# Optimization experiments

Measured on AMD Instinct MI355X. Metric: run time of the kernel, lower is better.

Reference implementation:

```python
import jax, jax.numpy as jnp
import numpy as np

D, H, K = 384, 6, 8

def _ln(x, g, b, eps=1e-5):
    mu = jnp.mean(x, axis=-1, keepdims=True)
    var = jnp.mean((x - mu) ** 2, axis=-1, keepdims=True)
    return (x - mu) * jax.lax.rsqrt(var + eps) * g + b

def setup_inputs() -> dict:
    key = jax.random.key(0)
    ks = jax.random.split(key, 20)
    B, N = 4, 2048
    s = 0.02
    inp = {
        'x': jax.random.normal(ks[0], (B, N, D), jnp.float32),
        'knn_index': jax.random.randint(ks[1], (B * K * N,), 0, B * N, jnp.int64),
        'ln1_g': jnp.ones((D,), jnp.float32),
        'ln1_b': jnp.zeros((D,), jnp.float32),
        'w_qkv': jax.random.normal(ks[2], (D, 3 * D), jnp.float32) * s,
        'w_proj': jax.random.normal(ks[3], (D, D), jnp.float32) * s,
        'b_proj': jnp.zeros((D,), jnp.float32),
        'w_knn': jax.random.normal(ks[4], (2 * D, D), jnp.float32) * s,
        'b_knn': jnp.zeros((D,), jnp.float32),
        'w_g1': jax.random.normal(ks[5], (2 * D, D), jnp.float32) * s,
        'b_g1': jnp.zeros((D,), jnp.float32),
        'w_g2': jax.random.normal(ks[6], (D, D), jnp.float32) * s,
        'b_g2': jnp.zeros((D,), jnp.float32),
        'ln2_g': jnp.ones((D,), jnp.float32),
        'ln2_b': jnp.zeros((D,), jnp.float32),
        'w_fc1': jax.random.normal(ks[7], (D, 4 * D), jnp.float32) * s,
        'b_fc1': jnp.zeros((4 * D,), jnp.float32),
        'w_fc2': jax.random.normal(ks[8], (4 * D, D), jnp.float32) * s,
        'b_fc2': jnp.zeros((D,), jnp.float32),
    }
    return inp

def reference(x, knn_index, ln1_g, ln1_b, w_qkv, w_proj, b_proj, w_knn, b_knn,
              w_g1, b_g1, w_g2, b_g2, ln2_g, ln2_b, w_fc1, b_fc1, w_fc2, b_fc2):
    B, N, _ = x.shape
    hd = D // H
    scale = hd ** -0.5
    nx = _ln(x, ln1_g, ln1_b)
    # --- self attention ---
    qkv = (nx @ w_qkv).reshape(B, N, 3, H, hd).transpose(2, 0, 3, 1, 4)  # [3,B,H,N,hd]
    q, k, v = qkv[0], qkv[1], qkv[2]
    attn = jax.nn.softmax(jnp.einsum('bhnd,bhmd->bhnm', q * scale, k), axis=-1)
    attn_out = jnp.einsum('bhnm,bhmd->bhnd', attn, v).transpose(0, 2, 1, 3).reshape(B, N, D)
    attn_out = attn_out @ w_proj + b_proj
    # --- EdgeConv-style graph feature: gather-concat-MLP-maxpool ---
    feat = nx.reshape(B * N, D)[knn_index].reshape(B, K, N, D)
    xe = jnp.broadcast_to(nx[:, None], (B, K, N, D))
    gf = jnp.concatenate([feat - xe, xe], axis=-1)  # [B,K,N,2D]
    knn_out = jnp.max(jax.nn.leaky_relu(gf @ w_knn + b_knn, 0.2), axis=1)  # [B,N,D]
    # --- salience gate ---
    gi = jnp.concatenate([attn_out, knn_out], axis=-1)
    gate = jax.nn.sigmoid(jax.nn.gelu(gi @ w_g1 + b_g1, approximate=False) @ w_g2 + b_g2)
    fused = (1 - gate) * attn_out + gate * knn_out
    x = x + fused
    # --- FFN ---
    h = jax.nn.gelu(_ln(x, ln2_g, ln2_b) @ w_fc1 + b_fc1, approximate=False)
    x = x + (h @ w_fc2 + b_fc2)
    return x
```

## Files before the change

### kernel.cpp

```cpp
#include <hip/hip_runtime.h>
#include <math.h>

typedef unsigned short u16;
typedef __attribute__((ext_vector_type(8))) short short8;
typedef __attribute__((ext_vector_type(4))) float floatx4;
typedef __attribute__((ext_vector_type(16))) float floatx16;
typedef __attribute__((ext_vector_type(4))) short sh4v;
typedef __attribute__((ext_vector_type(2))) unsigned uint2v;

union sh4u { sh4v v; u16 u[4]; };
union sh8u { short8 v; u16 u[8]; };
union sh8w { short8 v; unsigned w[4]; };

__device__ __forceinline__ floatx4 mfma16(short8 a, short8 b, floatx4 c) {
  return __builtin_amdgcn_mfma_f32_16x16x32_bf16(a, b, c, 0, 0, 0);
}
__device__ __forceinline__ floatx16 mfma32(short8 a, short8 b, floatx16 c) {
  return __builtin_amdgcn_mfma_f32_32x32x16_bf16(a, b, c, 0, 0, 0);
}

__device__ __forceinline__ floatx4 zero4() {
  floatx4 z = {0.f, 0.f, 0.f, 0.f};
  return z;
}
__device__ __forceinline__ floatx16 zero16() {
  floatx16 z;
#pragma unroll
  for (int i = 0; i < 16; i++) z[i] = 0.f;
  return z;
}

__device__ __forceinline__ float hexp2(float x) {
  return __builtin_amdgcn_exp2f(x);
}

__device__ __forceinline__ u16 f2b(float f) {
  union { float f; unsigned u; } v; v.f = f;
  unsigned u = v.u;
  return (u16)((u + 0x7FFFu + ((u >> 16) & 1u)) >> 16);
}

__device__ __forceinline__ float b2f(u16 u) {
  union { unsigned u; float f; } v; v.u = ((unsigned)u) << 16;
  return v.f;
}

__device__ __forceinline__ float blo(unsigned w) {
  union { unsigned u; float f; } v; v.u = w << 16;
  return v.f;
}
__device__ __forceinline__ float bhi(unsigned w) {
  union { unsigned u; float f; } v; v.u = w & 0xFFFF0000u;
  return v.f;
}

__device__ __forceinline__ float gelu_exact(float x) {
  return 0.5f * x * (1.f + erff(x * 0.70710678118654752440f));
}

__device__ __forceinline__ unsigned pack2(float a, float b) {
  return (unsigned)f2b(a) | ((unsigned)f2b(b) << 16);
}

__device__ __forceinline__ unsigned permpack(float p0, float p1) {
  return __builtin_amdgcn_perm(__float_as_uint(p1), __float_as_uint(p0), 0x07060302u);
}

__global__ __launch_bounds__(256) void tcln_kernel(
    const float* __restrict__ p0, const float* __restrict__ p1,
    const float* __restrict__ p2, const float* __restrict__ p3,
    const float* __restrict__ p4, const float* __restrict__ p5,
    const float* __restrict__ wknn,
    u16* __restrict__ o0, u16* __restrict__ o1, u16* __restrict__ o2,
    u16* __restrict__ o3, u16* __restrict__ o4, u16* __restrict__ o5,
    u16* __restrict__ wcT,
    const float* __restrict__ x, const float* __restrict__ g,
    const float* __restrict__ bia, u16* __restrict__ nx) {
  __shared__ u16 L[64][66];
  int t = blockIdx.x, tid = threadIdx.x;
  if (t >= 612) {
    int wave = tid >> 6, lane = tid & 63;
    int row = (t - 612) * 4 + wave;
    const float* xr = x + (size_t)row * 384;
    float v[6];
    float s = 0.f;
#pragma unroll
    for (int j = 0; j < 6; j++) { v[j] = xr[lane + 64 * j]; s += v[j]; }
#pragma unroll
    for (int off = 32; off > 0; off >>= 1) s += __shfl_xor(s, off);
    float mu = s * (1.f / 384.f);
    float ss = 0.f;
#pragma unroll
    for (int j = 0; j < 6; j++) { float d = v[j] - mu; ss += d * d; }
#pragma unroll
    for (int off = 32; off > 0; off >>= 1) ss += __shfl_xor(ss, off);
    float rstd = rsqrtf(ss * (1.f / 384.f) + 1e-5f);
    u16* orow = nx + (size_t)row * 384;
#pragma unroll
    for (int j = 0; j < 6; j++) {
      int d = lane + 64 * j;
      orow[d] = f2b((v[j] - mu) * rstd * g[d] + bia[d]);
    }
    return;
  }
  if (t >= 540) {
    t -= 540;
    int tk = t / 12, tn = t % 12;
    int k0 = tk * 64, j0 = tn * 64;
#pragma unroll
    for (int i = 0; i < 4; i++) {
      int c = tid + 256 * i;
      int r = c >> 4, c4 = (c & 15) * 4;
      floatx4 v;
      if (j0 < 384) {
        v = *(const floatx4*)(wknn + (size_t)(k0 + r) * 384 + j0 + c4);
      } else {
        floatx4 a = *(const floatx4*)(wknn + (size_t)(384 + k0 + r) * 384 + (j0 - 384) + c4);
        floatx4 b = *(const floatx4*)(wknn + (size_t)(k0 + r) * 384 + (j0 - 384) + c4);
        v = a - b;
      }
      *(unsigned*)&L[r][c4]     = pack2(v[0], v[1]);
      *(unsigned*)&L[r][c4 + 2] = pack2(v[2], v[3]);
    }
    __syncthreads();
#pragma unroll
    for (int i = 0; i < 2; i++) {
      int c = tid + 256 * i;
      int nn = c >> 3, k8 = (c & 7) * 8;
      sh8u pk;
#pragma unroll
      for (int j = 0; j < 8; j++) pk.u[j] = L[k8 + j][nn];
      *(short8*)(wcT + (size_t)(j0 + nn) * 384 + k0 + k8) = pk.v;
    }
    return;
  }
  const float* src; u16* dst; int Kd, Nd, tk, tn;
  if      (t < 108) { src = p0; dst = o0; Kd = 384;  Nd = 1152; tk = t / 18; tn = t % 18; }
  else if (t < 144) { src = p1; dst = o1; Kd = 384;  Nd = 384;  t -= 108; tk = t / 6;  tn = t % 6; }
  else if (t < 216) { src = p2; dst = o2; Kd = 768;  Nd = 384;  t -= 144; tk = t / 6;  tn = t % 6; }
  else if (t < 252) { src = p3; dst = o3; Kd = 384;  Nd = 384;  t -= 216; tk = t / 6;  tn = t % 6; }
  else if (t < 396) { src = p4; dst = o4; Kd = 384;  Nd = 1536; t -= 252; tk = t / 24; tn = t % 24; }
  else              { src = p5; dst = o5; Kd = 1536; Nd = 384;  t -= 396; tk = t / 6;  tn = t % 6; }
  int k0 = tk * 64, n0 = tn * 64;
#pragma unroll
  for (int i = 0; i < 4; i++) {
    int c = tid + 256 * i;
    int r = c >> 4, c4 = (c & 15) * 4;
    floatx4 v = *(const floatx4*)(src + (size_t)(k0 + r) * Nd + n0 + c4);
    *(unsigned*)&L[r][c4]     = pack2(v[0], v[1]);
    *(unsigned*)&L[r][c4 + 2] = pack2(v[2], v[3]);
  }
  __syncthreads();
#pragma unroll
  for (int i = 0; i < 2; i++) {
    int c = tid + 256 * i;
    int nn = c >> 3, k8 = (c & 7) * 8;
    sh8u pk;
#pragma unroll
    for (int j = 0; j < 8; j++) pk.u[j] = L[k8 + j][nn];
    *(short8*)(dst + (size_t)(n0 + nn) * Kd + k0 + k8) = pk.v;
  }
}

__global__ __launch_bounds__(256) void lnb_kernel(const u16* __restrict__ x,
                                                  const float* __restrict__ g,
                                                  const float* __restrict__ bia,
                                                  u16* __restrict__ out) {
  int wave = threadIdx.x >> 6, lane = threadIdx.x & 63;
  int row = blockIdx.x * 4 + wave;
  const u16* xr = x + (size_t)row * 384;
  float v[6];
  float s = 0.f;
#pragma unroll
  for (int j = 0; j < 6; j++) { v[j] = b2f(xr[lane + 64 * j]); s += v[j]; }
#pragma unroll
  for (int off = 32; off > 0; off >>= 1) s += __shfl_xor(s, off);
  float mu = s * (1.f / 384.f);
  float ss = 0.f;
#pragma unroll
  for (int j = 0; j < 6; j++) { float d = v[j] - mu; ss += d * d; }
#pragma unroll
  for (int off = 32; off > 0; off >>= 1) ss += __shfl_xor(ss, off);
  float rstd = rsqrtf(ss * (1.f / 384.f) + 1e-5f);
  u16* orow = out + (size_t)row * 384;
#pragma unroll
  for (int j = 0; j < 6; j++) {
    int d = lane + 64 * j;
    orow[d] = f2b((v[j] - mu) * rstd * g[d] + bia[d]);
  }
}

template <int EPI>
__global__ __launch_bounds__(256) void gemm64_kernel(
    const u16* __restrict__ A0, const u16* __restrict__ A1, int Ksplit,
    const u16* __restrict__ BwT, const u16* __restrict__ BwT2, int N, int K,
    const float* __restrict__ bias,
    float* __restrict__ outF, u16* __restrict__ outB, u16* __restrict__ outB2,
    const u16* __restrict__ eA16, const u16* __restrict__ eK16,
    const float* __restrict__ eX, u16* __restrict__ outV) {
  __shared__ u16 As[64][72];
  __shared__ u16 Bs[128][72];
  int tid = threadIdx.x;
  int lane = tid & 63, w = tid >> 6, quad = lane >> 4, l16 = lane & 15;
  int n0 = blockIdx.x * 128, m0 = blockIdx.y * 64;
  int ra = tid >> 3, ca = (tid & 7) * 8;
  const u16* Bsrc = BwT;
  int nbase = n0;
  if (EPI == 8 && n0 >= 1152) { Bsrc = BwT2; nbase = n0 - 1152; }
  floatx4 acc[4][2];
#pragma unroll
  for (int i = 0; i < 4; i++)
#pragma unroll
    for (int j = 0; j < 2; j++) acc[i][j] = zero4();

  short8 pa[2], pb[4];
  auto loadAB = [&](int k0) {
    const u16* Ap;
    int kk, sA;
    if (k0 < Ksplit) { Ap = A0; kk = k0; sA = Ksplit; }
    else             { Ap = A1; kk = k0 - Ksplit; sA = K - Ksplit; }
    pa[0] = *(const short8*)(Ap + (size_t)(m0 + ra) * sA + kk + ca);
    pa[1] = *(const short8*)(Ap + (size_t)(m0 + ra + 32) * sA + kk + ca);
#pragma unroll
    for (int i = 0; i < 4; i++)
      pb[i] = *(const short8*)(Bsrc + (size_t)(nbase + ra + 32 * i) * K + k0 + ca);
  };
  loadAB(0);
  int iters = K >> 6;
  for (int kt = 0; kt < iters; kt++) {
    __syncthreads();
    *(short8*)&As[ra][ca] = pa[0];
    *(short8*)&As[ra + 32][ca] = pa[1];
#pragma unroll
    for (int i = 0; i < 4; i++) *(short8*)&Bs[ra + 32 * i][ca] = pb[i];
    __syncthreads();
    if (kt + 1 < iters) loadAB((kt + 1) * 64);
#pragma unroll
    for (int kh = 0; kh < 2; kh++) {
      short8 af[4], bfr[2];
#pragma unroll
      for (int mt = 0; mt < 4; mt++)
        af[mt] = *(const short8*)&As[mt * 16 + l16][kh * 32 + quad * 8];
#pragma unroll
      for (int nt = 0; nt < 2; nt++)
        bfr[nt] = *(const short8*)&Bs[w * 32 + nt * 16 + l16][kh * 32 + quad * 8];
#pragma unroll
      for (int mt = 0; mt < 4; mt++)
#pragma unroll
        for (int nt = 0; nt < 2; nt++)
          acc[mt][nt] = mfma16(af[mt], bfr[nt], acc[mt][nt]);
    }
  }

#pragma unroll
  for (int mt = 0; mt < 4; mt++)
#pragma unroll
    for (int nt = 0; nt < 2; nt++) {
      int col = n0 + w * 32 + nt * 16 + l16;
      int row0 = m0 + mt * 16 + quad * 4;
      if (EPI == 8) {
        if (col < 1152) {
          float sc = (col < 384) ? 0.18033688011112042f : 1.f;
          sh4u pk;
#pragma unroll
          for (int r = 0; r < 4; r++) {
            u16 bv = f2b(acc[mt][nt][r] * sc);
            outB[(size_t)(row0 + r) * 1152 + col] = bv;
            pk.u[r] = bv;
          }
          if (col >= 768) {
            int b = row0 >> 11, n = row0 & 2047;
            int hd = col - 768;
            *(sh4v*)(outV + ((size_t)(b * 6 + (hd >> 6)) * 64 + (hd & 63)) * 2048 + n) = pk.v;
          }
        } else {
#pragma unroll
          for (int r = 0; r < 4; r++)
            outB2[(size_t)(row0 + r) * 768 + (col - 1152)] = f2b(acc[mt][nt][r]);
        }
      } else {
#pragma unroll
        for (int r = 0; r < 4; r++) {
          size_t rc = (size_t)(row0 + r) * N + col;
          float v = acc[mt][nt][r];
          if (EPI == 3) {
            outB[rc] = f2b(gelu_exact(v + bias[col]));
          } else if (EPI == 4) {
            float gte = 1.f / (1.f + hexp2(-1.44269504088896f * (v + bias[col])));
            float fu = (1.f - gte) * b2f(eA16[rc]) + gte * b2f(eK16[rc]);
            outB[rc] = f2b(eX[rc] + fu);
          } else if (EPI == 7) {
            outF[rc] = v + bias[col] + b2f(eA16[rc]);
          }
        }
      }
    }
}

__global__ __launch_bounds__(256) void attnknn_kernel(
    const u16* __restrict__ qkv, const u16* __restrict__ Vt,
    u16* __restrict__ OPb, float* __restrict__ LS,
    const u16* __restrict__ GBb, const int* __restrict__ kidx,
    const float* __restrict__ bknn, u16* __restrict__ knn_bf) {
  __shared__ u16 Ks[2][64][72];
  __shared__ u16 Vts[2][64][72];
  int bid = blockIdx.x, tid = threadIdx.x;
  int lane = tid & 63, w = tid >> 6;
  if (bid >= 768) {
    int row = (bid - 768) * 4 + w;
    int b = row >> 11, n = row & 2047;
    const unsigned* browp = (const unsigned*)(GBb + (size_t)row * 768 + 384);
    uint2v bw01 = *(const uint2v*)(browp + 2 * lane);
    unsigned bw2 = browp[128 + lane];
    floatx4 bk4 = *(const floatx4*)(bknn + 4 * lane);
    float bk40 = bknn[256 + 2 * lane], bk41 = bknn[256 + 2 * lane + 1];
    int gi[8];
#pragma unroll
    for (int kk = 0; kk < 8; kk++) gi[kk] = kidx[(b * 8 + kk) * 2048 + n];
    float mx[6];
#pragma unroll
    for (int e = 0; e < 6; e++) mx[e] = -1e30f;
#pragma unroll
    for (int kk = 0; kk < 8; kk++) {
      const unsigned* gp = (const unsigned*)(GBb + (size_t)gi[kk] * 768);
      uint2v g01 = *(const uint2v*)(gp + 2 * lane);
      unsigned g2 = gp[128 + lane];
      mx[0] = fmaxf(mx[0], blo(g01[0]));
      mx[1] = fmaxf(mx[1], bhi(g01[0]));
      mx[2] = fmaxf(mx[2], blo(g01[1]));
      mx[3] = fmaxf(mx[3], bhi(g01[1]));
      mx[4] = fmaxf(mx[4], blo(g2));
      mx[5] = fmaxf(mx[5], bhi(g2));
    }
    float vv[6];
    vv[0] = mx[0] + blo(bw01[0]) + bk4[0];
    vv[1] = mx[1] + bhi(bw01[0]) + bk4[1];
    vv[2] = mx[2] + blo(bw01[1]) + bk4[2];
    vv[3] = mx[3] + bhi(bw01[1]) + bk4[3];
    vv[4] = mx[4] + blo(bw2) + bk40;
    vv[5] = mx[5] + bhi(bw2) + bk41;
#pragma unroll
    for (int e = 0; e < 6; e++) vv[e] = fmaxf(vv[e], 0.2f * vv[e]);
    unsigned* op = (unsigned*)(knn_bf + (size_t)row * 384);
    uint2v ow;
    ow[0] = pack2(vv[0], vv[1]);
    ow[1] = pack2(vv[2], vv[3]);
    *(uint2v*)(op + 2 * lane) = ow;
    op[128 + lane] = pack2(vv[4], vv[5]);
    return;
  }
  int vb = (bid & 7) * 96 + (bid >> 3);
  int split = vb / 384;
  int rr = vb - split * 384;
  int bh = rr >> 4, b = bh / 6, h = bh % 6;
  int q0 = (rr & 15) * 128;
  int ql = lane & 31, h5 = lane >> 5;
  const u16* qbase = qkv + (size_t)b * 2048 * 1152 + h * 64;
  const u16* kbase = qbase + 384 + (size_t)split * 1024 * 1152;
  const u16* vtb = Vt + (size_t)bh * 64 * 2048 + split * 1024;
  int qrow = q0 + w * 32 + ql;
  short8 qB[4];
#pragma unroll
  for (int s = 0; s < 4; s++)
    qB[s] = *(const short8*)(qbase + (size_t)qrow * 1152 + s * 16 + h5 * 8);
  floatx16 O[2];
  O[0] = zero16(); O[1] = zero16();
  float accLs = 0.f;

  int rb = tid >> 3, c8 = (tid & 7) * 8;
  short8 rk[2], rv[2];
  rk[0] = *(const short8*)(kbase + (size_t)rb * 1152 + c8);
  rk[1] = *(const short8*)(kbase + (size_t)(rb + 32) * 1152 + c8);
  rv[0] = *(const short8*)(vtb + (size_t)rb * 2048 + c8);
  rv[1] = *(const short8*)(vtb + (size_t)(rb + 32) * 2048 + c8);

  int cur = 0;
  for (int kt = 0; kt < 16; kt++) {
    *(short8*)&Ks[cur][rb][c8] = rk[0];
    *(short8*)&Ks[cur][rb + 32][c8] = rk[1];
    *(short8*)&Vts[cur][rb][c8] = rv[0];
    *(short8*)&Vts[cur][rb + 32][c8] = rv[1];
    __syncthreads();
    if (kt < 15) {
      int key0 = (kt + 1) * 64;
      rk[0] = *(const short8*)(kbase + (size_t)(key0 + rb) * 1152 + c8);
      rk[1] = *(const short8*)(kbase + (size_t)(key0 + rb + 32) * 1152 + c8);
      rv[0] = *(const short8*)(vtb + (size_t)rb * 2048 + key0 + c8);
      rv[1] = *(const short8*)(vtb + (size_t)(rb + 32) * 2048 + key0 + c8);
    }
#pragma unroll
    for (int t = 0; t < 2; t++) {
      floatx16 st = zero16();
#pragma unroll
      for (int s = 0; s < 4; s++) {
        short8 aK = *(const short8*)&Ks[cur][32 * t + ql][16 * s + 8 * h5];
        st = mfma32(aK, qB[s], st);
      }
      unsigned W[8];
#pragma unroll
      for (int j = 0; j < 8; j++) {
        float e0 = hexp2(st[2 * j]), e1 = hexp2(st[2 * j + 1]);
        accLs += e0 + e1;
        W[j] = permpack(e0, e1);
      }
#pragma unroll
      for (int c = 0; c < 2; c++) {
        int kk = 2 * t + c;
        uint2v s0 = __builtin_amdgcn_permlane32_swap(W[4 * c], W[4 * c + 2], false, false);
        uint2v s1 = __builtin_amdgcn_permlane32_swap(W[4 * c + 1], W[4 * c + 3], false, false);
        sh8w pb_;
        pb_.w[0] = s0[0];
        pb_.w[1] = s1[0];
        pb_.w[2] = s0[1];
        pb_.w[3] = s1[1];
        short8 aV0 = *(const short8*)&Vts[cur][ql][16 * kk + 8 * h5];
        short8 aV1 = *(const short8*)&Vts[cur][32 + ql][16 * kk + 8 * h5];
        O[0] = mfma32(aV0, pb_.v, O[0]);
        O[1] = mfma32(aV1, pb_.v, O[1]);
      }
    }
    cur ^= 1;
  }
  u16* orow = OPb + (size_t)split * 8192 * 384 + (size_t)(b * 2048 + qrow) * 384 + h * 64;
#pragma unroll
  for (int d = 0; d < 2; d++)
#pragma unroll
    for (int rq = 0; rq < 4; rq++) {
      sh4u pk;
#pragma unroll
      for (int r3 = 0; r3 < 4; r3++) pk.u[r3] = f2b(O[d][4 * rq + r3]);
      *(sh4v*)(orow + 32 * d + 8 * rq + 4 * h5) = pk.v;
    }
  uint2v sw = __builtin_amdgcn_permlane32_swap(__float_as_uint(accLs), __float_as_uint(accLs),
                                               false, false);
  if (lane < 32) LS[split * 8192 + b * 2048 + qrow] = accLs + __uint_as_float(sw[1]);
}

__global__ __launch_bounds__(256) void projc_kernel(
    const u16* __restrict__ OPb, const float* __restrict__ LS,
    const u16* __restrict__ BwT, const float* __restrict__ bias,
    u16* __restrict__ outB) {
  __shared__ u16 As[64][72];
  __shared__ u16 Bs[128][72];
  int tid = threadIdx.x;
  int lane = tid & 63, w = tid >> 6, quad = lane >> 4, l16 = lane & 15;
  int n0 = blockIdx.x * 128, m0 = blockIdx.y * 64;
  int ra = tid >> 3, ca = (tid & 7) * 8;
  const size_t SP = (size_t)8192 * 384;
  floatx4 acc[4][2];
#pragma unroll
  for (int i = 0; i < 4; i++)
#pragma unroll
    for (int j = 0; j < 2; j++) acc[i][j] = zero4();

  short8 pa[2], pb[4];
  auto loadAB = [&](int k0) {
#pragma unroll
    for (int i = 0; i < 2; i++) {
      const u16* p = OPb + (size_t)(m0 + ra + 32 * i) * 384 + k0 + ca;
      sh8u a0, a1, pk;
      a0.v = *(const short8*)p;
      a1.v = *(const short8*)(p + SP);
#pragma unroll
      for (int j = 0; j < 8; j++)
        pk.u[j] = f2b(b2f(a0.u[j]) + b2f(a1.u[j]));
      pa[i] = pk.v;
    }
#pragma unroll
    for (int i = 0; i < 4; i++)
      pb[i] = *(const short8*)(BwT + (size_t)(n0 + ra + 32 * i) * 384 + k0 + ca);
  };
  loadAB(0);
  for (int kt = 0; kt < 6; kt++) {
    __syncthreads();
    *(short8*)&As[ra][ca] = pa[0];
    *(short8*)&As[ra + 32][ca] = pa[1];
#pragma unroll
    for (int i = 0; i < 4; i++) *(short8*)&Bs[ra + 32 * i][ca] = pb[i];
    __syncthreads();
    if (kt < 5) loadAB((kt + 1) * 64);
#pragma unroll
    for (int kh = 0; kh < 2; kh++) {
      short8 af[4], bfr[2];
#pragma unroll
      for (int mt = 0; mt < 4; mt++)
        af[mt] = *(const short8*)&As[mt * 16 + l16][kh * 32 + quad * 8];
#pragma unroll
      for (int nt = 0; nt < 2; nt++)
        bfr[nt] = *(const short8*)&Bs[w * 32 + nt * 16 + l16][kh * 32 + quad * 8];
#pragma unroll
      for (int mt = 0; mt < 4; mt++)
#pragma unroll
        for (int nt = 0; nt < 2; nt++)
          acc[mt][nt] = mfma16(af[mt], bfr[nt], acc[mt][nt]);
    }
  }
#pragma unroll
  for (int mt = 0; mt < 4; mt++) {
    int row0 = m0 + mt * 16 + quad * 4;
    float rl[4];
#pragma unroll
    for (int r = 0; r < 4; r++) {
      int gr = row0 + r;
      rl[r] = 1.f / (LS[gr] + LS[8192 + gr]);
    }
#pragma unroll
    for (int nt = 0; nt < 2; nt++) {
      int col = n0 + w * 32 + nt * 16 + l16;
#pragma unroll
      for (int r = 0; r < 4; r++)
        outB[(size_t)(row0 + r) * 384 + col] = f2b(acc[mt][nt][r] * rl[r] + bias[col]);
    }
  }
}

extern "C" void kernel_launch(void* const* d_in, const int* in_sizes, int n_in,
                              void* d_out, int out_size, void* d_ws, size_t ws_size,
                              hipStream_t stream) {
  const float* x    = (const float*)d_in[0];
  const int* kidx   = (const int*)d_in[1];
  const float* ln1g = (const float*)d_in[2];
  const float* ln1b = (const float*)d_in[3];
  const float* wqkv = (const float*)d_in[4];
  const float* wproj= (const float*)d_in[5];
  const float* bproj= (const float*)d_in[6];
  const float* wknn = (const float*)d_in[7];
  const float* bknn = (const float*)d_in[8];
  const float* wg1  = (const float*)d_in[9];
  const float* bg1  = (const float*)d_in[10];
  const float* wg2  = (const float*)d_in[11];
  const float* bg2  = (const float*)d_in[12];
  const float* ln2g = (const float*)d_in[13];
  const float* ln2b = (const float*)d_in[14];
  const float* wfc1 = (const float*)d_in[15];
  const float* bfc1 = (const float*)d_in[16];
  const float* wfc2 = (const float*)d_in[17];
  const float* bfc2 = (const float*)d_in[18];
  float* out = (float*)d_out;

  const int M = 8192;
  char* ws = (char*)d_ws;
  size_t off = 0;
  auto alloc = [&](size_t bytes) -> char* {
    char* p = ws + off;
    off += (bytes + 255) & ~(size_t)255;
    return p;
  };
  u16* nx_bf    = (u16*)alloc((size_t)M * 384 * 2);
  u16* qkv_bf   = (u16*)alloc((size_t)M * 1152 * 2);
  u16* attn_bf  = (u16*)alloc((size_t)M * 384 * 2);
  u16* GBb      = (u16*)alloc((size_t)M * 768 * 2);
  u16* knn_bf   = (u16*)alloc((size_t)M * 384 * 2);
  u16* x2b      = (u16*)alloc((size_t)M * 384 * 2);
  u16* t1_bf    = (u16*)alloc((size_t)M * 384 * 2);
  u16* nx2_bf   = (u16*)alloc((size_t)M * 384 * 2);
  u16* Vt_b     = (u16*)alloc((size_t)24 * 64 * 2048 * 2);
  u16* OPb      = (u16*)alloc((size_t)2 * M * 384 * 2);
  float* LS     = (float*)alloc((size_t)2 * M * 4);
  u16* wqkvT    = (u16*)alloc((size_t)1152 * 384 * 2);
  u16* wprojT   = (u16*)alloc(384 * 384 * 2);
  u16* wcT      = (u16*)alloc((size_t)768 * 384 * 2);
  u16* wg1T     = (u16*)alloc((size_t)384 * 768 * 2);
  u16* wg2T     = (u16*)alloc(384 * 384 * 2);
  u16* wfc1T    = (u16*)alloc((size_t)1536 * 384 * 2);
  u16* wfc2T    = (u16*)alloc((size_t)384 * 1536 * 2);
  u16* h_bf     = qkv_bf;

  tcln_kernel<<<2660, 256, 0, stream>>>(wqkv, wproj, wg1, wg2, wfc1, wfc2, wknn,
                                        wqkvT, wprojT, wg1T, wg2T, wfc1T, wfc2T, wcT,
                                        x, ln1g, ln1b, nx_bf);
  gemm64_kernel<8><<<dim3(15, 128), 256, 0, stream>>>(nx_bf, nx_bf, 384, wqkvT, wcT, 1920, 384,
                                                      nullptr, nullptr, qkv_bf, GBb,
                                                      nullptr, nullptr, nullptr, Vt_b);
  attnknn_kernel<<<2816, 256, 0, stream>>>(qkv_bf, Vt_b, OPb, LS,
                                           GBb, kidx, bknn, knn_bf);
  projc_kernel<<<dim3(3, 128), 256, 0, stream>>>(OPb, LS, wprojT, bproj, attn_bf);
  gemm64_kernel<3><<<dim3(3, 128), 256, 0, stream>>>(attn_bf, knn_bf, 384, wg1T, nullptr, 384, 768,
                                                     bg1, nullptr, t1_bf, nullptr,
                                                     nullptr, nullptr, nullptr, nullptr);
  gemm64_kernel<4><<<dim3(3, 128), 256, 0, stream>>>(t1_bf, t1_bf, 384, wg2T, nullptr, 384, 384,
                                                     bg2, nullptr, x2b, nullptr,
                                                     attn_bf, knn_bf, x, nullptr);
  lnb_kernel<<<2048, 256, 0, stream>>>(x2b, ln2g, ln2b, nx2_bf);
  gemm64_kernel<3><<<dim3(12, 128), 256, 0, stream>>>(nx2_bf, nx2_bf, 384, wfc1T, nullptr, 1536, 384,
                                                      bfc1, nullptr, h_bf, nullptr,
                                                      nullptr, nullptr, nullptr, nullptr);
  gemm64_kernel<7><<<dim3(3, 128), 256, 0, stream>>>(h_bf, h_bf, 1536, wfc2T, nullptr, 384, 1536,
                                                     bfc2, out, nullptr, nullptr,
                                                     x2b, nullptr, nullptr, nullptr);
  (void)in_sizes; (void)n_in; (void)out_size; (void)ws_size;
}
```

Baseline: 255.6 us.

## Remove split-K in attention and normalize output inside attention kernel

Attention blocks now process all 2048 keys in one block instead of splitting keys across two blocks, so 384 attention blocks replace 768. Softmax normalization moves into the attention epilogue, which drops the LS buffer and the second partial-output buffer. The projection kernel no longer reads and sums two partial outputs, cutting its memory traffic. The cost is fewer attention blocks and a longer serial key loop per block, which lowers parallelism on a device with many compute units.

```diff
diff --git a/kernel.cpp b/kernel.cpp
--- a/kernel.cpp
+++ b/kernel.cpp
@@ -299,15 +299,15 @@
 
 __global__ __launch_bounds__(256) void attnknn_kernel(
     const u16* __restrict__ qkv, const u16* __restrict__ Vt,
-    u16* __restrict__ OPb, float* __restrict__ LS,
+    u16* __restrict__ OPb,
     const u16* __restrict__ GBb, const int* __restrict__ kidx,
     const float* __restrict__ bknn, u16* __restrict__ knn_bf) {
   __shared__ u16 Ks[2][64][72];
   __shared__ u16 Vts[2][64][72];
   int bid = blockIdx.x, tid = threadIdx.x;
   int lane = tid & 63, w = tid >> 6;
-  if (bid >= 768) {
-    int row = (bid - 768) * 4 + w;
+  if (bid >= 384) {
+    int row = (bid - 384) * 4 + w;
     int b = row >> 11, n = row & 2047;
     const unsigned* browp = (const unsigned*)(GBb + (size_t)row * 768 + 384);
     uint2v bw01 = *(const uint2v*)(browp + 2 * lane);
@@ -349,15 +349,13 @@
     op[128 + lane] = pack2(vv[4], vv[5]);
     return;
   }
-  int vb = (bid & 7) * 96 + (bid >> 3);
-  int split = vb / 384;
-  int rr = vb - split * 384;
-  int bh = rr >> 4, b = bh / 6, h = bh % 6;
-  int q0 = (rr & 15) * 128;
+  int vb = (bid & 7) * 48 + (bid >> 3);
+  int bh = vb >> 4, b = bh / 6, h = bh % 6;
+  int q0 = (vb & 15) * 128;
   int ql = lane & 31, h5 = lane >> 5;
   const u16* qbase = qkv + (size_t)b * 2048 * 1152 + h * 64;
-  const u16* kbase = qbase + 384 + (size_t)split * 1024 * 1152;
-  const u16* vtb = Vt + (size_t)bh * 64 * 2048 + split * 1024;
+  const u16* kbase = qbase + 384;
+  const u16* vtb = Vt + (size_t)bh * 64 * 2048;
   int qrow = q0 + w * 32 + ql;
   short8 qB[4];
 #pragma unroll
@@ -375,13 +373,13 @@
   rv[1] = *(const short8*)(vtb + (size_t)(rb + 32) * 2048 + c8);
 
   int cur = 0;
-  for (int kt = 0; kt < 16; kt++) {
+  for (int kt = 0; kt < 32; kt++) {
     *(short8*)&Ks[cur][rb][c8] = rk[0];
     *(short8*)&Ks[cur][rb + 32][c8] = rk[1];
     *(short8*)&Vts[cur][rb][c8] = rv[0];
     *(short8*)&Vts[cur][rb + 32][c8] = rv[1];
     __syncthreads();
-    if (kt < 15) {
+    if (kt < 31) {
       int key0 = (kt + 1) * 64;
       rk[0] = *(const short8*)(kbase + (size_t)(key0 + rb) * 1152 + c8);
       rk[1] = *(const short8*)(kbase + (size_t)(key0 + rb + 32) * 1152 + c8);
@@ -421,23 +419,22 @@
     }
     cur ^= 1;
   }
-  u16* orow = OPb + (size_t)split * 8192 * 384 + (size_t)(b * 2048 + qrow) * 384 + h * 64;
+  float rs = accLs + __shfl_xor(accLs, 32);
+  float ri = 1.f / rs;
+  u16* orow = OPb + (size_t)(b * 2048 + qrow) * 384 + h * 64;
 #pragma unroll
   for (int d = 0; d < 2; d++)
 #pragma unroll
     for (int rq = 0; rq < 4; rq++) {
       sh4u pk;
 #pragma unroll
-      for (int r3 = 0; r3 < 4; r3++) pk.u[r3] = f2b(O[d][4 * rq + r3]);
+      for (int r3 = 0; r3 < 4; r3++) pk.u[r3] = f2b(O[d][4 * rq + r3] * ri);
       *(sh4v*)(orow + 32 * d + 8 * rq + 4 * h5) = pk.v;
     }
-  uint2v sw = __builtin_amdgcn_permlane32_swap(__float_as_uint(accLs), __float_as_uint(accLs),
-                                               false, false);
-  if (lane < 32) LS[split * 8192 + b * 2048 + qrow] = accLs + __uint_as_float(sw[1]);
 }
 
 __global__ __launch_bounds__(256) void projc_kernel(
-    const u16* __restrict__ OPb, const float* __restrict__ LS,
+    const u16* __restrict__ OPb,
     const u16* __restrict__ BwT, const float* __restrict__ bias,
     u16* __restrict__ outB) {
   __shared__ u16 As[64][72];
@@ -446,7 +443,6 @@
   int lane = tid & 63, w = tid >> 6, quad = lane >> 4, l16 = lane & 15;
   int n0 = blockIdx.x * 128, m0 = blockIdx.y * 64;
   int ra = tid >> 3, ca = (tid & 7) * 8;
-  const size_t SP = (size_t)8192 * 384;
   floatx4 acc[4][2];
 #pragma unroll
   for (int i = 0; i < 4; i++)
@@ -455,17 +451,8 @@
 
   short8 pa[2], pb[4];
   auto loadAB = [&](int k0) {
-#pragma unroll
-    for (int i = 0; i < 2; i++) {
-      const u16* p = OPb + (size_t)(m0 + ra + 32 * i) * 384 + k0 + ca;
-      sh8u a0, a1, pk;
-      a0.v = *(const short8*)p;
-      a1.v = *(const short8*)(p + SP);
-#pragma unroll
-      for (int j = 0; j < 8; j++)
-        pk.u[j] = f2b(b2f(a0.u[j]) + b2f(a1.u[j]));
-      pa[i] = pk.v;
-    }
+    pa[0] = *(const short8*)(OPb + (size_t)(m0 + ra) * 384 + k0 + ca);
+    pa[1] = *(const short8*)(OPb + (size_t)(m0 + ra + 32) * 384 + k0 + ca);
 #pragma unroll
     for (int i = 0; i < 4; i++)
       pb[i] = *(const short8*)(BwT + (size_t)(n0 + ra + 32 * i) * 384 + k0 + ca);
@@ -498,18 +485,12 @@
 #pragma unroll
   for (int mt = 0; mt < 4; mt++) {
     int row0 = m0 + mt * 16 + quad * 4;
-    float rl[4];
-#pragma unroll
-    for (int r = 0; r < 4; r++) {
-      int gr = row0 + r;
-      rl[r] = 1.f / (LS[gr] + LS[8192 + gr]);
-    }
 #pragma unroll
     for (int nt = 0; nt < 2; nt++) {
       int col = n0 + w * 32 + nt * 16 + l16;
 #pragma unroll
       for (int r = 0; r < 4; r++)
-        outB[(size_t)(row0 + r) * 384 + col] = f2b(acc[mt][nt][r] * rl[r] + bias[col]);
+        outB[(size_t)(row0 + r) * 384 + col] = f2b(acc[mt][nt][r] + bias[col]);
     }
   }
 }
@@ -555,8 +536,7 @@
   u16* t1_bf    = (u16*)alloc((size_t)M * 384 * 2);
   u16* nx2_bf   = (u16*)alloc((size_t)M * 384 * 2);
   u16* Vt_b     = (u16*)alloc((size_t)24 * 64 * 2048 * 2);
-  u16* OPb      = (u16*)alloc((size_t)2 * M * 384 * 2);
-  float* LS     = (float*)alloc((size_t)2 * M * 4);
+  u16* OPb      = (u16*)alloc((size_t)M * 384 * 2);
   u16* wqkvT    = (u16*)alloc((size_t)1152 * 384 * 2);
   u16* wprojT   = (u16*)alloc(384 * 384 * 2);
   u16* wcT      = (u16*)alloc((size_t)768 * 384 * 2);
@@ -572,9 +552,9 @@
   gemm64_kernel<8><<<dim3(15, 128), 256, 0, stream>>>(nx_bf, nx_bf, 384, wqkvT, wcT, 1920, 384,
                                                       nullptr, nullptr, qkv_bf, GBb,
                                                       nullptr, nullptr, nullptr, Vt_b);
-  attnknn_kernel<<<2816, 256, 0, stream>>>(qkv_bf, Vt_b, OPb, LS,
+  attnknn_kernel<<<2432, 256, 0, stream>>>(qkv_bf, Vt_b, OPb,
                                            GBb, kidx, bknn, knn_bf);
-  projc_kernel<<<dim3(3, 128), 256, 0, stream>>>(OPb, LS, wprojT, bproj, attn_bf);
+  projc_kernel<<<dim3(3, 128), 256, 0, stream>>>(OPb, wprojT, bproj, attn_bf);
   gemm64_kernel<3><<<dim3(3, 128), 256, 0, stream>>>(attn_bf, knn_bf, 384, wg1T, nullptr, 384, 768,
                                                      bg1, nullptr, t1_bf, nullptr,
                                                      nullptr, nullptr, nullptr, nullptr);
```

Result: slower. 266.0 us (+4.1%).
